# Performance work log

Hardware: AMD Instinct MI355X
Metric: run time of the kernel (lower is better)

## Reference

```python
import jax, jax.numpy as jnp
import numpy as np

N = 8192
D = 2048      # input_dim
DH = 1024     # input_dim // r
DO = 1024     # output_dim

def setup_inputs() -> dict:
    key = jax.random.key(0)
    ks = jax.random.split(key, 11)
    s_in = 1.0 / np.sqrt(D)
    s_h = 1.0 / np.sqrt(DH)
    return {
        "O0": jax.random.normal(ks[0], (N, D), dtype=jnp.float32),
        "Ww": jax.random.uniform(ks[1], (DH, D), jnp.float32, -s_in, s_in),
        "Wb": jax.random.uniform(ks[2], (DH,), jnp.float32, -s_in, s_in),
        "Uw": jax.random.uniform(ks[3], (DH, D), jnp.float32, -s_in, s_in),
        "Ub": jax.random.uniform(ks[4], (DH,), jnp.float32, -s_in, s_in),
        "Hw": jax.random.uniform(ks[5], (DH, D), jnp.float32, -s_in, s_in),
        "Hb": jax.random.uniform(ks[6], (DH,), jnp.float32, -s_in, s_in),
        "fc0w": jax.random.uniform(ks[7], (D, DH), jnp.float32, -s_h, s_h),
        "fc0b": jax.random.uniform(ks[8], (D,), jnp.float32, -s_h, s_h),
        "fc1w": jax.random.uniform(ks[9], (DO, D), jnp.float32, -s_in, s_in),
        "fc1b": jax.random.uniform(ks[10], (DO,), jnp.float32, -s_in, s_in),
    }

def reference(O0, Ww, Wb, Uw, Ub, Hw, Hb, fc0w, fc0b, fc1w, fc1b):
    q = O0 @ Ww.T + Wb              # [N, DH]
    k = O0 @ Uw.T + Ub              # [N, DH]
    v = O0 @ Hw.T + Hb              # [N, DH]
    scores = q @ k.T                # [N, N], unscaled as in the original
    R1 = jax.nn.softmax(scores, axis=1)
    ctx = R1 @ v                    # [N, DH]
    O1 = O0 + (ctx @ fc0w.T + fc0b) # residual, [N, D]
    O2 = O1 @ fc1w.T + fc1b         # [N, DO]
    return (O1, O2)
```

## Files before the change

### kernel.cpp

```cpp
#include <hip/hip_runtime.h>
#include <cstdint>
#include <cstddef>

typedef _Float16 f16;
typedef _Float16 f16x8 __attribute__((ext_vector_type(8)));
typedef _Float16 f16x4 __attribute__((ext_vector_type(4)));
typedef float    f32x4 __attribute__((ext_vector_type(4)));

template <int V> struct IC { static constexpr int v = V; };

__global__ __launch_bounds__(256) void cvt_f32_f16(const float* __restrict__ in,
                                                   f16* __restrict__ out, int n) {
  int i = (blockIdx.x * 256 + threadIdx.x) * 4;
  if (i < n) {
    float4 v = *(const float4*)(in + i);
    f16x4 h; h[0] = (f16)v.x; h[1] = (f16)v.y; h[2] = (f16)v.z; h[3] = (f16)v.w;
    *(f16x4*)(out + i) = h;
  }
}

__global__ __launch_bounds__(256) void transpose_f16(const f16* __restrict__ in,
                                                     int ldi,
                                                     f16* __restrict__ out,
                                                     int R, int C) {
  __shared__ f16 tile[64][65];
  const int r0 = blockIdx.y * 64, c0 = blockIdx.x * 64;
  const int t = threadIdx.x;
#pragma unroll
  for (int p = 0; p < 2; p++) {
    int s = t + p * 256;
    int r = s >> 3, q = s & 7;
    f16x8 v = *(const f16x8*)(in + (size_t)(r0 + r) * ldi + c0 + q * 8);
#pragma unroll
    for (int e = 0; e < 8; e++) tile[r][q * 8 + e] = v[e];
  }
  __syncthreads();
#pragma unroll
  for (int p = 0; p < 2; p++) {
    int s = t + p * 256;
    int r = s >> 3, q = s & 7;
    f16x8 v;
#pragma unroll
    for (int e = 0; e < 8; e++) v[e] = tile[q * 8 + e][r];
    *(f16x8*)(out + (size_t)(c0 + r) * R + r0 + q * 8) = v;
  }
}

template <int MODE>
__global__ __launch_bounds__(512, 2) void gemm256(
    const f16* __restrict__ A, const f16* __restrict__ B,
    int M, int N, int K, int lda, int ldb,
    const float* __restrict__ bias,
    f16* __restrict__ outH, int ldo,
    float* __restrict__ statsM, float* __restrict__ statsS, int sld,
    const float* __restrict__ alphaT,
    const float* __restrict__ resid, int ldr,
    float* __restrict__ outF, int ldof) {
  __shared__ f16 lA[2][2][128 * 64];
  __shared__ f16 lB[2][2][128 * 64];
  __shared__ float lAl[2][256];

  const int t = threadIdx.x;
  const int wave = t >> 6, lane = t & 63;
  const int wr = wave >> 2, wc = wave & 3;
  const int quad = lane >> 4, l16 = lane & 15;
  const int rc = lane >> 3;
  const int kcs = (lane & 7) ^ rc;

  const int nwg = gridDim.x * gridDim.y;
  const int bid = blockIdx.y * gridDim.x + blockIdx.x;
  const int sb = (bid & 7) * (nwg >> 3) + (bid >> 3);
  const int bx = sb % gridDim.x, by = sb / gridDim.x;
  const int m0 = by * 256, n0 = bx * 256;
  const int nk = K >> 6;

  const f16* Abase = A + (size_t)m0 * lda;
  const f16* Bbase = B + (size_t)n0 * ldb;

  auto stageA = [&](int tau, int h) {
    if (tau >= nk) return;
    const f16* src = Abase + (size_t)(h * 128 + rc) * lda + tau * 64 + kcs * 8;
    f16* dstu = &lA[tau & 1][h][0];
#pragma unroll
    for (int j = 0; j < 2; j++) {
      const int sl = j * 8 + wave;
      __builtin_amdgcn_global_load_lds(
          (const __attribute__((address_space(1))) void*)(src + (size_t)sl * 8 * lda),
          (__attribute__((address_space(3))) void*)(dstu + sl * 512), 16, 0, 0);
    }
  };
  auto stageB = [&](int tau, int h) {
    if (tau >= nk) return;
    const f16* src = Bbase + (size_t)(h * 128 + rc) * ldb + tau * 64 + kcs * 8;
    f16* dstu = &lB[tau & 1][h][0];
#pragma unroll
    for (int j = 0; j < 2; j++) {
      const int sl = j * 8 + wave;
      __builtin_amdgcn_global_load_lds(
          (const __attribute__((address_space(1))) void*)(src + (size_t)sl * 8 * ldb),
          (__attribute__((address_space(3))) void*)(dstu + sl * 512), 16, 0, 0);
    }
  };
  auto stageAl = [&](int tau) {
    if constexpr (MODE == 2) {
      if (tau >= nk) return;
      __builtin_amdgcn_global_load_lds(
          (const __attribute__((address_space(1))) void*)(alphaT + (size_t)tau * M + m0 + lane * 4),
          (__attribute__((address_space(3))) void*)(&lAl[tau & 1][0]), 16, 0, 0);
    }
  };

  f32x4 acc[2][4][2][2];
#pragma unroll
  for (int mh = 0; mh < 2; mh++)
#pragma unroll
    for (int i = 0; i < 4; i++)
#pragma unroll
      for (int nh = 0; nh < 2; nh++)
#pragma unroll
        for (int j = 0; j < 2; j++)
#pragma unroll
          for (int e = 0; e < 4; e++) acc[mh][i][nh][j][e] = 0.0f;

  f16x8 af[4][2];
  f16x8 bf[2][2][2];

  auto readA = [&](auto BUFC, auto MHC) {
    constexpr int buf = decltype(BUFC)::v;
    constexpr int mh = decltype(MHC)::v;
#pragma unroll
    for (int i = 0; i < 4; i++) {
      const int r = i * 32 + wr * 16 + l16;
#pragma unroll
      for (int s = 0; s < 2; s++) {
        const int p = ((s * 4 + quad) ^ (l16 & 7)) * 8;
        af[i][s] = *(const f16x8*)(&lA[buf][mh][r * 64 + p]);
      }
      if constexpr (MODE == 2) {
        const f16 ah = (f16)lAl[buf][mh * 128 + r];
        af[i][0] = af[i][0] * ah;
        af[i][1] = af[i][1] * ah;
      }
    }
  };
  auto readB = [&](auto BUFC, auto NHC) {
    constexpr int buf = decltype(BUFC)::v;
    constexpr int nh = decltype(NHC)::v;
    const int hb = wc >> 1;
#pragma unroll
    for (int j = 0; j < 2; j++) {
      const int r = (wc & 1) * 64 + nh * 32 + j * 16 + l16;
#pragma unroll
      for (int s = 0; s < 2; s++) {
        const int p = ((s * 4 + quad) ^ (l16 & 7)) * 8;
        bf[nh][j][s] = *(const f16x8*)(&lB[buf][hb][r * 64 + p]);
      }
    }
  };
  auto mfmaQ = [&](auto MHC, auto NHC) {
    constexpr int mh = decltype(MHC)::v;
    constexpr int nh = decltype(NHC)::v;
    __builtin_amdgcn_s_setprio(1);
#pragma unroll
    for (int i = 0; i < 4; i++)
#pragma unroll
      for (int j = 0; j < 2; j++)
#pragma unroll
        for (int s = 0; s < 2; s++)
          acc[mh][i][nh][j] = __builtin_amdgcn_mfma_f32_16x16x32_f16(
              af[i][s], bf[nh][j][s], acc[mh][i][nh][j], 0, 0, 0);
    __builtin_amdgcn_s_setprio(0);
  };

  auto tile4 = [&](auto BUFC, int tt, bool dr) {
    readA(BUFC, IC<0>{});
    readB(BUFC, IC<0>{});
    stageA(tt + 1, 1);
    stageAl(tt + 1);
    __builtin_amdgcn_s_barrier();
    asm volatile("s_waitcnt lgkmcnt(0)" ::: "memory");
    mfmaQ(IC<0>{}, IC<0>{});
    __builtin_amdgcn_s_barrier();
    readB(BUFC, IC<1>{});
    stageA(tt + 2, 0);
    __builtin_amdgcn_s_barrier();
    asm volatile("s_waitcnt lgkmcnt(0)" ::: "memory");
    mfmaQ(IC<0>{}, IC<1>{});
    __builtin_amdgcn_s_barrier();
    readA(BUFC, IC<1>{});
    stageB(tt + 2, 0);
    __builtin_amdgcn_s_barrier();
    asm volatile("s_waitcnt lgkmcnt(0)" ::: "memory");
    mfmaQ(IC<1>{}, IC<1>{});
    __builtin_amdgcn_s_barrier();
    stageB(tt + 2, 1);
    __builtin_amdgcn_s_barrier();
    mfmaQ(IC<1>{}, IC<0>{});
    if (dr) { asm volatile("s_waitcnt vmcnt(0)" ::: "memory"); }
    else    { asm volatile("s_waitcnt vmcnt(6)" ::: "memory"); }
    __builtin_amdgcn_s_barrier();
  };

  stageA(0, 0); stageB(0, 0); stageB(0, 1); stageA(0, 1);
  stageAl(0);
  stageA(1, 0); stageB(1, 0); stageB(1, 1);
  asm volatile("s_waitcnt vmcnt(6)" ::: "memory");
  __builtin_amdgcn_s_barrier();

  for (int tt = 0; tt < nk; tt += 2) {
    const bool dr = (tt + 2 >= nk);
    tile4(IC<0>{}, tt, dr);
    tile4(IC<1>{}, tt + 1, dr);
  }

  const int colb = n0 + wc * 64 + l16;
  float bv[4];
  if constexpr (MODE == 0 || MODE == 3 || MODE == 4) {
#pragma unroll
    for (int c = 0; c < 4; c++) bv[c] = bias[colb + c * 16];
  }
#pragma unroll
  for (int mh = 0; mh < 2; mh++) {
#pragma unroll
    for (int i = 0; i < 4; i++) {
#pragma unroll
      for (int e = 0; e < 4; e++) {
        const int gr = m0 + mh * 128 + i * 32 + wr * 16 + quad * 4 + e;
        const float v0 = acc[mh][i][0][0][e];
        const float v1 = acc[mh][i][0][1][e];
        const float v2 = acc[mh][i][1][0][e];
        const float v3 = acc[mh][i][1][1][e];
        if constexpr (MODE == 1) {
          float mx = fmaxf(fmaxf(v0, v1), fmaxf(v2, v3));
          mx = fmaxf(mx, __shfl_xor(mx, 1));
          mx = fmaxf(mx, __shfl_xor(mx, 2));
          mx = fmaxf(mx, __shfl_xor(mx, 4));
          mx = fmaxf(mx, __shfl_xor(mx, 8));
          float e0 = __expf(v0 - mx);
          float e1 = __expf(v1 - mx);
          float e2 = __expf(v2 - mx);
          float e3 = __expf(v3 - mx);
          float sm = (e0 + e1) + (e2 + e3);
          sm += __shfl_xor(sm, 1);
          sm += __shfl_xor(sm, 2);
          sm += __shfl_xor(sm, 4);
          sm += __shfl_xor(sm, 8);
          if (l16 == 0) {
            statsM[(size_t)gr * sld + (bx * 4 + wc)] = mx;
            statsS[(size_t)gr * sld + (bx * 4 + wc)] = sm;
          }
          f16* rp = outH + (size_t)gr * ldo + colb;
          rp[0]  = (f16)e0;
          rp[16] = (f16)e1;
          rp[32] = (f16)e2;
          rp[48] = (f16)e3;
        } else if constexpr (MODE == 0) {
          f16* rp = outH + (size_t)gr * ldo + colb;
          rp[0]  = (f16)(v0 + bv[0]);
          rp[16] = (f16)(v1 + bv[1]);
          rp[32] = (f16)(v2 + bv[2]);
          rp[48] = (f16)(v3 + bv[3]);
        } else if constexpr (MODE == 2) {
          f16* rp = outH + (size_t)gr * ldo + colb;
          rp[0]  = (f16)v0;
          rp[16] = (f16)v1;
          rp[32] = (f16)v2;
          rp[48] = (f16)v3;
        } else if constexpr (MODE == 3) {
          float* rf = outF + (size_t)gr * ldof + colb;
          const float* rr = resid + (size_t)gr * ldr + colb;
          f16* rh = outH + (size_t)gr * ldo + colb;
          float o0 = v0 + bv[0] + rr[0];
          float o1 = v1 + bv[1] + rr[16];
          float o2 = v2 + bv[2] + rr[32];
          float o3 = v3 + bv[3] + rr[48];
          rf[0] = o0; rf[16] = o1; rf[32] = o2; rf[48] = o3;
          rh[0] = (f16)o0; rh[16] = (f16)o1; rh[32] = (f16)o2; rh[48] = (f16)o3;
        } else {
          float* rf = outF + (size_t)gr * ldof + colb;
          rf[0]  = v0 + bv[0];
          rf[16] = v1 + bv[1];
          rf[32] = v2 + bv[2];
          rf[48] = v3 + bv[3];
        }
      }
    }
  }
}

template <int MODE>
__global__ __launch_bounds__(512, 2) void gemmN128(
    const f16* __restrict__ A, const f16* __restrict__ B,
    int M, int N, int K, int lda, int ldb,
    const float* __restrict__ bias,
    f16* __restrict__ outH, int ldo,
    const float* __restrict__ alphaT,
    float* __restrict__ outF, int ldof) {
  __shared__ f16 lA[2][2][128 * 64];
  __shared__ f16 lB[2][128 * 64];
  __shared__ float lAl[2][256];

  const int t = threadIdx.x;
  const int wave = t >> 6, lane = t & 63;
  const int wr = wave >> 1, wc = wave & 1;
  const int quad = lane >> 4, l16 = lane & 15;
  const int rc = lane >> 3;
  const int kcs = (lane & 7) ^ rc;

  const int nwg = gridDim.x * gridDim.y;
  const int bid = blockIdx.y * gridDim.x + blockIdx.x;
  const int sb = (bid & 7) * (nwg >> 3) + (bid >> 3);
  const int bx = sb % gridDim.x, by = sb / gridDim.x;
  const int m0 = by * 256, n0 = bx * 128;
  const int nk = K >> 6;

  const f16* Abase = A + (size_t)m0 * lda;
  const f16* Bbase = B + (size_t)n0 * ldb;

  auto stageA = [&](int tau, int h) {
    if (tau >= nk) return;
    const f16* src = Abase + (size_t)(h * 128 + rc) * lda + tau * 64 + kcs * 8;
    f16* dstu = &lA[tau & 1][h][0];
#pragma unroll
    for (int j = 0; j < 2; j++) {
      const int sl = j * 8 + wave;
      __builtin_amdgcn_global_load_lds(
          (const __attribute__((address_space(1))) void*)(src + (size_t)sl * 8 * lda),
          (__attribute__((address_space(3))) void*)(dstu + sl * 512), 16, 0, 0);
    }
  };
  auto stageB = [&](int tau) {
    if (tau >= nk) return;
    const f16* src = Bbase + (size_t)rc * ldb + tau * 64 + kcs * 8;
    f16* dstu = &lB[tau & 1][0];
#pragma unroll
    for (int j = 0; j < 2; j++) {
      const int sl = j * 8 + wave;
      __builtin_amdgcn_global_load_lds(
          (const __attribute__((address_space(1))) void*)(src + (size_t)sl * 8 * ldb),
          (__attribute__((address_space(3))) void*)(dstu + sl * 512), 16, 0, 0);
    }
  };
  auto stageAl = [&](int tau) {
    if constexpr (MODE == 2) {
      if (tau >= nk) return;
      __builtin_amdgcn_global_load_lds(
          (const __attribute__((address_space(1))) void*)(alphaT + (size_t)tau * M + m0 + lane * 4),
          (__attribute__((address_space(3))) void*)(&lAl[tau & 1][0]), 16, 0, 0);
    }
  };

  f32x4 acc[4][2][2];
#pragma unroll
  for (int i = 0; i < 4; i++)
#pragma unroll
    for (int nh = 0; nh < 2; nh++)
#pragma unroll
      for (int j = 0; j < 2; j++)
#pragma unroll
        for (int e = 0; e < 4; e++) acc[i][nh][j][e] = 0.0f;

  f16x8 af[4][2];
  f16x8 bf[2][2][2];
  const int ha = wr >> 1;

  auto readA = [&](auto BUFC) {
    constexpr int buf = decltype(BUFC)::v;
#pragma unroll
    for (int i = 0; i < 4; i++) {
      const int r = (wr & 1) * 64 + i * 16 + l16;
#pragma unroll
      for (int s = 0; s < 2; s++) {
        const int p = ((s * 4 + quad) ^ (l16 & 7)) * 8;
        af[i][s] = *(const f16x8*)(&lA[buf][ha][r * 64 + p]);
      }
      if constexpr (MODE == 2) {
        const f16 ah = (f16)lAl[buf][wr * 64 + i * 16 + l16];
        af[i][0] = af[i][0] * ah;
        af[i][1] = af[i][1] * ah;
      }
    }
  };
  auto readB = [&](auto BUFC, auto NHC) {
    constexpr int buf = decltype(BUFC)::v;
    constexpr int nh = decltype(NHC)::v;
#pragma unroll
    for (int j = 0; j < 2; j++) {
      const int r = wc * 64 + nh * 32 + j * 16 + l16;
#pragma unroll
      for (int s = 0; s < 2; s++) {
        const int p = ((s * 4 + quad) ^ (l16 & 7)) * 8;
        bf[nh][j][s] = *(const f16x8*)(&lB[buf][r * 64 + p]);
      }
    }
  };
  auto mfmaQ = [&](auto NHC) {
    constexpr int nh = decltype(NHC)::v;
    __builtin_amdgcn_s_setprio(1);
#pragma unroll
    for (int i = 0; i < 4; i++)
#pragma unroll
      for (int j = 0; j < 2; j++)
#pragma unroll
        for (int s = 0; s < 2; s++)
          acc[i][nh][j] = __builtin_amdgcn_mfma_f32_16x16x32_f16(
              af[i][s], bf[nh][j][s], acc[i][nh][j], 0, 0, 0);
    __builtin_amdgcn_s_setprio(0);
  };

  auto tile2 = [&](auto BUFC, int tt, bool dr) {
    readA(BUFC);
    readB(BUFC, IC<0>{});
    readB(BUFC, IC<1>{});
    stageA(tt + 1, 1);
    stageAl(tt + 1);
    __builtin_amdgcn_s_barrier();
    asm volatile("s_waitcnt lgkmcnt(0)" ::: "memory");
    mfmaQ(IC<0>{});
    __builtin_amdgcn_s_barrier();
    stageA(tt + 2, 0);
    stageB(tt + 2);
    __builtin_amdgcn_s_barrier();
    mfmaQ(IC<1>{});
    if (dr) { asm volatile("s_waitcnt vmcnt(0)" ::: "memory"); }
    else    { asm volatile("s_waitcnt vmcnt(4)" ::: "memory"); }
    __builtin_amdgcn_s_barrier();
  };

  stageA(0, 0); stageB(0); stageA(0, 1); stageAl(0);
  stageA(1, 0); stageB(1);
  asm volatile("s_waitcnt vmcnt(4)" ::: "memory");
  __builtin_amdgcn_s_barrier();

  for (int tt = 0; tt < nk; tt += 2) {
    const bool dr = (tt + 2 >= nk);
    tile2(IC<0>{}, tt, dr);
    tile2(IC<1>{}, tt + 1, dr);
  }

  float bv[2][2];
  if constexpr (MODE == 4) {
#pragma unroll
    for (int nh = 0; nh < 2; nh++)
#pragma unroll
      for (int j = 0; j < 2; j++)
        bv[nh][j] = bias[n0 + wc * 64 + nh * 32 + j * 16 + l16];
  }
#pragma unroll
  for (int i = 0; i < 4; i++) {
#pragma unroll
    for (int e = 0; e < 4; e++) {
      const int gr = m0 + wr * 64 + i * 16 + quad * 4 + e;
#pragma unroll
      for (int nh = 0; nh < 2; nh++) {
#pragma unroll
        for (int j = 0; j < 2; j++) {
          const int col = n0 + wc * 64 + nh * 32 + j * 16 + l16;
          const float v = acc[i][nh][j][e];
          if constexpr (MODE == 2) {
            outH[(size_t)gr * ldo + col] = (f16)v;
          } else {
            outF[(size_t)gr * ldof + col] = v + bv[nh][j];
          }
        }
      }
    }
  }
}

__global__ __launch_bounds__(256) void alpha_from_stats(
    const float* __restrict__ sM, const float* __restrict__ sS,
    float* __restrict__ aT, int rows) {
  __shared__ float alph[128][65];
  const int t = threadIdx.x;
  const int r = t >> 2, j = t & 3;
  const int row = blockIdx.x * 64 + r;
  const float* pm = sM + (size_t)row * 128 + j * 32;
  const float* ps = sS + (size_t)row * 128 + j * 32;
  float mv[32];
  float mx = -1e30f;
#pragma unroll
  for (int c = 0; c < 32; c++) { mv[c] = pm[c]; mx = fmaxf(mx, mv[c]); }
  mx = fmaxf(mx, __shfl_xor(mx, 1));
  mx = fmaxf(mx, __shfl_xor(mx, 2));
  float ev[32];
  float sum = 0.0f;
#pragma unroll
  for (int c = 0; c < 32; c++) {
    ev[c] = __expf(mv[c] - mx);
    sum += ev[c] * ps[c];
  }
  sum += __shfl_xor(sum, 1);
  sum += __shfl_xor(sum, 2);
  const float rl = 1.0f / sum;
#pragma unroll
  for (int c = 0; c < 32; c++) alph[j * 32 + c][r] = ev[c] * rl;
  __syncthreads();
  const int wid = t >> 6, rr = t & 63;
#pragma unroll
  for (int c = 0; c < 32; c++) {
    const int tg = c * 4 + wid;
    aT[(size_t)tg * rows + blockIdx.x * 64 + rr] = alph[tg][rr];
  }
}

extern "C" void kernel_launch(void* const* d_in, const int* in_sizes, int n_in,
                              void* d_out, int out_size, void* d_ws, size_t ws_size,
                              hipStream_t stream) {
  const float* O0   = (const float*)d_in[0];
  const float* Ww   = (const float*)d_in[1];
  const float* Wb   = (const float*)d_in[2];
  const float* Uw   = (const float*)d_in[3];
  const float* Ub   = (const float*)d_in[4];
  const float* Hw   = (const float*)d_in[5];
  const float* Hb   = (const float*)d_in[6];
  const float* fc0w = (const float*)d_in[7];
  const float* fc0b = (const float*)d_in[8];
  const float* fc1w = (const float*)d_in[9];
  const float* fc1b = (const float*)d_in[10];

  const int N = 8192, D = 2048, DH = 1024, DO = 1024;
  const int NQKV = 3 * DH;

  char* w = (char*)d_ws;
  f16* Wwh   = (f16*)w; w += (size_t)DH * D * 2;
  f16* Uwh   = (f16*)w; w += (size_t)DH * D * 2;
  f16* Hwh   = (f16*)w; w += (size_t)DH * D * 2;
  f16* fc0wh = (f16*)w; w += (size_t)D * DH * 2;
  f16* fc1wh = (f16*)w; w += (size_t)DO * D * 2;
  float* aT  = (float*)w; w += (size_t)128 * N * 4;
  char* un = w; w += (size_t)N * DH * 2;
  float* statsM = (float*)un;
  float* statsS = statsM + (size_t)N * 128;
  f16* ctxh = (f16*)un;
  float* biasC = (float*)w; w += (size_t)NQKV * 4;
  w = (char*)(((uintptr_t)w + 255) & ~(uintptr_t)255);
  f16* Sb = (f16*)w;

  f16* oh   = (f16*)d_out;
  f16* qkv  = oh;
  f16* qh   = qkv;
  f16* kh   = qkv + DH;
  f16* vh   = qkv + 2 * DH;
  f16* O0h  = oh + (size_t)N * NQKV;
  f16* vT   = O0h + (size_t)N * D;
  f16* O1h  = Sb;

  {
    int n = DH * D;
    int grid = n / 1024;
    cvt_f32_f16<<<grid, 256, 0, stream>>>(Ww, Wwh, n);
    cvt_f32_f16<<<grid, 256, 0, stream>>>(Uw, Uwh, n);
    cvt_f32_f16<<<grid, 256, 0, stream>>>(Hw, Hwh, n);
    cvt_f32_f16<<<grid, 256, 0, stream>>>(fc0w, fc0wh, n);
    cvt_f32_f16<<<grid, 256, 0, stream>>>(fc1w, fc1wh, n);
    cvt_f32_f16<<<(N * D) / 1024, 256, 0, stream>>>(O0, O0h, N * D);
    hipMemcpyAsync(biasC,          Wb, DH * 4, hipMemcpyDeviceToDevice, stream);
    hipMemcpyAsync(biasC + DH,     Ub, DH * 4, hipMemcpyDeviceToDevice, stream);
    hipMemcpyAsync(biasC + 2 * DH, Hb, DH * 4, hipMemcpyDeviceToDevice, stream);
  }

  gemm256<0><<<dim3(NQKV / 256, N / 256), 512, 0, stream>>>(
      O0h, Wwh, N, NQKV, D, D, D, biasC,
      qkv, NQKV, nullptr, nullptr, 0, nullptr, nullptr, 0, nullptr, 0);

  transpose_f16<<<dim3(DH / 64, N / 64), 256, 0, stream>>>(vh, NQKV, vT, N, DH);

  gemm256<1><<<dim3(N / 256, N / 256), 512, 0, stream>>>(
      qh, kh, N, N, DH, NQKV, NQKV, nullptr, Sb, N,
      statsM, statsS, 128, nullptr, nullptr, 0, nullptr, 0);

  alpha_from_stats<<<N / 64, 256, 0, stream>>>(statsM, statsS, aT, N);

  gemmN128<2><<<dim3(DH / 128, N / 256), 512, 0, stream>>>(
      Sb, vT, N, DH, N, N, N, nullptr, ctxh, DH, aT, nullptr, 0);

  gemm256<3><<<dim3(D / 256, N / 256), 512, 0, stream>>>(
      ctxh, fc0wh, N, D, DH, DH, DH, fc0b, O1h, D,
      nullptr, nullptr, 0, nullptr, O0, D, (float*)d_out, D);

  gemmN128<4><<<dim3(DO / 128, N / 256), 512, 0, stream>>>(
      O1h, fc1wh, N, DO, D, D, D, fc1b, nullptr, 0, nullptr,
      (float*)d_out + (size_t)N * D, DO);
}
```

Baseline: 759.4 us.

## Batch weight conversions, use DPP reductions, vectorize softmax stores, retile QKV GEMM

The five weight fp32-to-fp16 conversion launches are merged into one kernel, which assumes the five fp16 weight buffers sit contiguously after Wwh. The softmax-stats GEMM replaces the first two shuffle-xor reduction steps with DPP row operations and writes packed f16x4 exponentials instead of strided scalar stores. The transpose gathers rows with a permuted index to match that new column layout. The QKV projection moves from the 256-wide to the 128-wide GEMM kernel with a new bias epilogue, which changes grid shape and occupancy.

New measurement: 763.3 us. About the same (+0.5%).

```diff
diff --git a/kernel.cpp b/kernel.cpp
--- a/kernel.cpp
+++ b/kernel.cpp
@@ -8,6 +8,14 @@
 typedef float    f32x4 __attribute__((ext_vector_type(4)));
 
 template <int V> struct IC { static constexpr int v = V; };
+
+template <int CTRL>
+__device__ __forceinline__ float dppf(float x) {
+  union { float f; int i; } u, r;
+  u.f = x;
+  r.i = __builtin_amdgcn_update_dpp(0, u.i, CTRL, 0xF, 0xF, true);
+  return r.f;
+}
 
 __global__ __launch_bounds__(256) void cvt_f32_f16(const float* __restrict__ in,
                                                    f16* __restrict__ out, int n) {
@@ -19,6 +27,20 @@
   }
 }
 
+__global__ __launch_bounds__(256) void cvt5_f32_f16(
+    const float* __restrict__ i0, const float* __restrict__ i1,
+    const float* __restrict__ i2, const float* __restrict__ i3,
+    const float* __restrict__ i4, f16* __restrict__ out, int nper) {
+  const int bpr = nper >> 10;
+  const int r = blockIdx.x / bpr;
+  const int b = blockIdx.x - r * bpr;
+  const float* in = r == 0 ? i0 : r == 1 ? i1 : r == 2 ? i2 : r == 3 ? i3 : i4;
+  int i = (b * 256 + threadIdx.x) * 4;
+  float4 v = *(const float4*)(in + i);
+  f16x4 h; h[0] = (f16)v.x; h[1] = (f16)v.y; h[2] = (f16)v.z; h[3] = (f16)v.w;
+  *(f16x4*)(out + (size_t)r * nper + i) = h;
+}
+
 __global__ __launch_bounds__(256) void transpose_f16(const f16* __restrict__ in,
                                                      int ldi,
                                                      f16* __restrict__ out,
@@ -30,7 +52,8 @@
   for (int p = 0; p < 2; p++) {
     int s = t + p * 256;
     int r = s >> 3, q = s & 7;
-    f16x8 v = *(const f16x8*)(in + (size_t)(r0 + r) * ldi + c0 + q * 8);
+    const int kl = ((r & 3) << 4) + (r >> 2);
+    f16x8 v = *(const f16x8*)(in + (size_t)(r0 + kl) * ldi + c0 + q * 8);
 #pragma unroll
     for (int e = 0; e < 8; e++) tile[r][q * 8 + e] = v[e];
   }
@@ -232,8 +255,8 @@
         const float v3 = acc[mh][i][1][1][e];
         if constexpr (MODE == 1) {
           float mx = fmaxf(fmaxf(v0, v1), fmaxf(v2, v3));
-          mx = fmaxf(mx, __shfl_xor(mx, 1));
-          mx = fmaxf(mx, __shfl_xor(mx, 2));
+          mx = fmaxf(mx, dppf<0xB1>(mx));
+          mx = fmaxf(mx, dppf<0x4E>(mx));
           mx = fmaxf(mx, __shfl_xor(mx, 4));
           mx = fmaxf(mx, __shfl_xor(mx, 8));
           float e0 = __expf(v0 - mx);
@@ -241,19 +264,17 @@
           float e2 = __expf(v2 - mx);
           float e3 = __expf(v3 - mx);
           float sm = (e0 + e1) + (e2 + e3);
-          sm += __shfl_xor(sm, 1);
-          sm += __shfl_xor(sm, 2);
+          sm += dppf<0xB1>(sm);
+          sm += dppf<0x4E>(sm);
           sm += __shfl_xor(sm, 4);
           sm += __shfl_xor(sm, 8);
           if (l16 == 0) {
             statsM[(size_t)gr * sld + (bx * 4 + wc)] = mx;
             statsS[(size_t)gr * sld + (bx * 4 + wc)] = sm;
           }
-          f16* rp = outH + (size_t)gr * ldo + colb;
-          rp[0]  = (f16)e0;
-          rp[16] = (f16)e1;
-          rp[32] = (f16)e2;
-          rp[48] = (f16)e3;
+          f16x4 pk;
+          pk[0] = (f16)e0; pk[1] = (f16)e1; pk[2] = (f16)e2; pk[3] = (f16)e3;
+          *(f16x4*)(outH + (size_t)gr * ldo + n0 + wc * 64 + l16 * 4) = pk;
         } else if constexpr (MODE == 0) {
           f16* rp = outH + (size_t)gr * ldo + colb;
           rp[0]  = (f16)(v0 + bv[0]);
@@ -439,7 +460,7 @@
   }
 
   float bv[2][2];
-  if constexpr (MODE == 4) {
+  if constexpr (MODE == 0 || MODE == 4) {
 #pragma unroll
     for (int nh = 0; nh < 2; nh++)
 #pragma unroll
@@ -459,6 +480,8 @@
           const float v = acc[i][nh][j][e];
           if constexpr (MODE == 2) {
             outH[(size_t)gr * ldo + col] = (f16)v;
+          } else if constexpr (MODE == 0) {
+            outH[(size_t)gr * ldo + col] = (f16)(v + bv[nh][j]);
           } else {
             outF[(size_t)gr * ldof + col] = v + bv[nh][j];
           }
@@ -547,22 +570,17 @@
   f16* O1h  = Sb;
 
   {
-    int n = DH * D;
-    int grid = n / 1024;
-    cvt_f32_f16<<<grid, 256, 0, stream>>>(Ww, Wwh, n);
-    cvt_f32_f16<<<grid, 256, 0, stream>>>(Uw, Uwh, n);
-    cvt_f32_f16<<<grid, 256, 0, stream>>>(Hw, Hwh, n);
-    cvt_f32_f16<<<grid, 256, 0, stream>>>(fc0w, fc0wh, n);
-    cvt_f32_f16<<<grid, 256, 0, stream>>>(fc1w, fc1wh, n);
+    int nper = DH * D;
+    cvt5_f32_f16<<<5 * (nper / 1024), 256, 0, stream>>>(
+        Ww, Uw, Hw, fc0w, fc1w, Wwh, nper);
     cvt_f32_f16<<<(N * D) / 1024, 256, 0, stream>>>(O0, O0h, N * D);
     hipMemcpyAsync(biasC,          Wb, DH * 4, hipMemcpyDeviceToDevice, stream);
     hipMemcpyAsync(biasC + DH,     Ub, DH * 4, hipMemcpyDeviceToDevice, stream);
     hipMemcpyAsync(biasC + 2 * DH, Hb, DH * 4, hipMemcpyDeviceToDevice, stream);
   }
 
-  gemm256<0><<<dim3(NQKV / 256, N / 256), 512, 0, stream>>>(
-      O0h, Wwh, N, NQKV, D, D, D, biasC,
-      qkv, NQKV, nullptr, nullptr, 0, nullptr, nullptr, 0, nullptr, 0);
+  gemmN128<0><<<dim3(NQKV / 128, N / 256), 512, 0, stream>>>(
+      O0h, Wwh, N, NQKV, D, D, D, biasC, qkv, NQKV, nullptr, nullptr, 0);
 
   transpose_f16<<<dim3(DH / 64, N / 64), 256, 0, stream>>>(vh, NQKV, vT, N, DH);
 
```
